# Kernel optimization log

Hardware: AMD Instinct MI355X
Metric: run time of the kernel (lower is better)

## Reference

```python
import jax, jax.numpy as jnp
import numpy as np

DIM = 1024
NUM_HEADS = 16
HEAD_DIM = DIM // NUM_HEADS
SCALE = DIM ** (-0.5)  # NOTE: original scales by full dim, not head_dim


def setup_inputs() -> dict:
    key = jax.random.key(0)
    ks = jax.random.split(key, 5)
    B, S = 2, 2048
    x = jax.random.normal(ks[0], (B, S, DIM), dtype=jnp.float32)
    w_qkv = jax.random.normal(ks[1], (DIM, 3 * DIM), dtype=jnp.float32) * (DIM ** -0.5)
    b_qkv = jax.random.normal(ks[2], (3 * DIM,), dtype=jnp.float32) * 0.02
    w_proj = jax.random.normal(ks[3], (DIM, DIM), dtype=jnp.float32) * (DIM ** -0.5)
    b_proj = jax.random.normal(ks[4], (DIM,), dtype=jnp.float32) * 0.02
    return {"x": x, "w_qkv": w_qkv, "b_qkv": b_qkv, "w_proj": w_proj, "b_proj": b_proj}


def reference(x, w_qkv, b_qkv, w_proj, b_proj):
    B, S, D = x.shape
    qkv = x @ w_qkv + b_qkv                                  # [B,S,3D]
    qkv = qkv.reshape(B, S, NUM_HEADS, 3 * HEAD_DIM).transpose(0, 2, 1, 3)  # [B,H,S,3hd]
    q, k, v = jnp.split(qkv, 3, axis=-1)                     # each [B,H,S,hd]
    attn = jnp.einsum("bhqd,bhkd->bhqk", q, k) * SCALE       # [B,H,S,S]
    attn = jax.nn.softmax(attn, axis=-1)
    out = jnp.einsum("bhqk,bhkd->bhqd", attn, v)             # [B,H,S,hd]
    out = out.transpose(0, 2, 1, 3).reshape(B, S, D)
    return out @ w_proj + b_proj
```

## Files before the change

kernel.cpp:

```cpp
#include <hip/hip_runtime.h>
#include <hip/hip_bf16.h>

#define DIM 1024
#define NH 16
#define HD 64
#define BB 2
#define SS 2048
#define MROWS (BB * SS)
#define SC_LOG2E 0.04508422002778011f

typedef unsigned short u16;
typedef unsigned int u32;
typedef __attribute__((ext_vector_type(8))) short short8;
typedef __attribute__((ext_vector_type(4))) float f32x4;

__device__ __forceinline__ u16 f2bf(float f) {
  union { float f; u32 u; } v; v.f = f;
  return (u16)((v.u + 0x7fffu + ((v.u >> 16) & 1u)) >> 16);
}

__device__ __forceinline__ u32 pack2bf(float a, float b) {
  union { __hip_bfloat162 h; u32 u; } cv;
  cv.h = __float22bfloat162_rn(make_float2(a, b));
  return cv.u;
}

__device__ __forceinline__ void async16(const u16* g, u16* l) {
  __builtin_amdgcn_global_load_lds(
      (const __attribute__((address_space(1))) void*)(const void*)g,
      (__attribute__((address_space(3))) void*)(void*)l, 16, 0, 0);
}

__device__ __forceinline__ short8 ld8(const u16* p) { return *(const short8*)p; }

__global__ void cvt_kernel(const float* __restrict__ in, u16* __restrict__ out, int n4) {
  int i = blockIdx.x * blockDim.x + threadIdx.x;
  if (i < n4) {
    float4 v = ((const float4*)in)[i];
    u32 lo = (u32)f2bf(v.x) | ((u32)f2bf(v.y) << 16);
    u32 hi = (u32)f2bf(v.z) | ((u32)f2bf(v.w) << 16);
    ((uint2*)out)[i] = make_uint2(lo, hi);
  }
}

__global__ void tconv_kernel(const float* __restrict__ in, u16* __restrict__ out, int R, int C) {
  __shared__ u16 t[64 * 65];
  int c0 = blockIdx.x * 64, r0 = blockIdx.y * 64;
  #pragma unroll
  for (int i = 0; i < 16; i++) {
    int j = i * 256 + threadIdx.x;
    int rr = j >> 6, cc = j & 63;
    t[rr * 65 + cc] = f2bf(in[(size_t)(r0 + rr) * C + c0 + cc]);
  }
  __syncthreads();
  #pragma unroll
  for (int i = 0; i < 16; i++) {
    int j = i * 256 + threadIdx.x;
    int oc = j >> 6, orr = j & 63;
    out[(size_t)(c0 + oc) * R + r0 + orr] = t[orr * 65 + oc];
  }
}

template <int MODE>
__global__ __launch_bounds__(256, 2) void gemm_bt(
    const u16* __restrict__ A, const u16* __restrict__ Bt,
    const float* __restrict__ bias, void* __restrict__ C,
    u16* __restrict__ vT, int M, int N, int K) {
  __shared__ __align__(16) u16 As[128 * 32];
  __shared__ __align__(16) u16 Bs[128 * 32];
  const int tid = threadIdx.x;
  const int w = tid >> 6, l = tid & 63;
  const int r = l & 15, q = l >> 4;
  const int m0 = blockIdx.y * 128, n0 = blockIdx.x * 128;
  const int qm = (w & 1) * 64, qn = (w >> 1) * 64;

  const size_t aoff = (size_t)(m0 + w * 16 + (l >> 2)) * K + (size_t)(l & 3) * 8;
  const size_t boff = (size_t)(n0 + w * 16 + (l >> 2)) * K + (size_t)(l & 3) * 8;
  u16* alds = &As[(w * 64 + l) * 8];
  u16* blds = &Bs[(w * 64 + l) * 8];

  f32x4 acc[4][4] = {};
  for (int k0 = 0; k0 < K; k0 += 32) {
    async16(A + aoff + k0, alds);
    async16(A + aoff + (size_t)64 * K + k0, alds + 2048);
    async16(Bt + boff + k0, blds);
    async16(Bt + boff + (size_t)64 * K + k0, blds + 2048);
    __syncthreads();
    short8 af[4], bfr[4];
    #pragma unroll
    for (int i = 0; i < 4; i++) af[i] = ld8(&As[(qm + i * 16 + r) * 32 + q * 8]);
    #pragma unroll
    for (int j = 0; j < 4; j++) bfr[j] = ld8(&Bs[(qn + j * 16 + r) * 32 + q * 8]);
    #pragma unroll
    for (int i = 0; i < 4; i++)
      #pragma unroll
      for (int j = 0; j < 4; j++)
        acc[i][j] = __builtin_amdgcn_mfma_f32_16x16x32_bf16(af[i], bfr[j], acc[i][j], 0, 0, 0);
    __syncthreads();
  }
  #pragma unroll
  for (int i = 0; i < 4; i++) {
    int ro = m0 + qm + i * 16 + q * 4;
    #pragma unroll
    for (int j = 0; j < 4; j++) {
      int col = n0 + qn + j * 16 + r;
      float bv = bias[col];
      float v0 = acc[i][j][0] + bv, v1 = acc[i][j][1] + bv;
      float v2 = acc[i][j][2] + bv, v3 = acc[i][j][3] + bv;
      if (MODE == 1) {
        float* out = (float*)C;
        out[(size_t)(ro + 0) * N + col] = v0;
        out[(size_t)(ro + 1) * N + col] = v1;
        out[(size_t)(ro + 2) * N + col] = v2;
        out[(size_t)(ro + 3) * N + col] = v3;
      } else {
        int h = col / 192, wi = col - h * 192;
        if (wi >= 128) {
          int bb = ro >> 11, s = ro & 2047, d = wi - 128;
          uint2 pk = make_uint2(pack2bf(v0, v1), pack2bf(v2, v3));
          *(uint2*)&vT[((size_t)((bb * NH + h) * HD + d)) * SS + s] = pk;
        } else {
          if (wi < 64) { v0 *= SC_LOG2E; v1 *= SC_LOG2E; v2 *= SC_LOG2E; v3 *= SC_LOG2E; }
          u16* qk2 = (u16*)C;
          qk2[(size_t)(ro + 0) * 2048 + h * 128 + wi] = f2bf(v0);
          qk2[(size_t)(ro + 1) * 2048 + h * 128 + wi] = f2bf(v1);
          qk2[(size_t)(ro + 2) * 2048 + h * 128 + wi] = f2bf(v2);
          qk2[(size_t)(ro + 3) * 2048 + h * 128 + wi] = f2bf(v3);
        }
      }
    }
  }
}

__global__ __launch_bounds__(256, 3) void attn4_kernel(
    const u16* __restrict__ qk2, const u16* __restrict__ vT,
    u16* __restrict__ attno) {
  __shared__ __align__(16) u16 Ks[128 * 64];
  __shared__ __align__(16) u16 Vs[64 * 128];
  __shared__ __align__(16) u16 pb[4][16 * 136];
  const int tid = threadIdx.x;
  const int w = tid >> 6, l = tid & 63;
  const int r = l & 15, q = l >> 4;
  const int b = blockIdx.z, h = blockIdx.y, q0 = blockIdx.x * 64;

  const u16* qb = qk2 + (size_t)b * SS * 2048;
  const u16* kB = qb + h * 128 + 64;
  const u16* vB = vT + (size_t)((b * NH + h) * HD) * SS;
  u16* pw = &pb[w][0];

  short8 qf[2];
  #pragma unroll
  for (int kq = 0; kq < 2; kq++)
    qf[kq] = ld8(qb + (size_t)(q0 + w * 16 + r) * 2048 + h * 128 + kq * 32 + q * 8);

  short8 ones;
  #pragma unroll
  for (int e = 0; e < 8; e++) ones[e] = (short)0x3F80;

  const int klrow = l >> 3;
  const int kchunk = (l & 7) ^ klrow;
  const int vlrow = l >> 4;
  const int vslot = l & 15;

  f32x4 oacc[4] = {};
  f32x4 dacc = {};

  for (int kv0 = 0; kv0 < SS; kv0 += 128) {
    #pragma unroll
    for (int t = 0; t < 4; t++) {
      int sl = (w * 4 + t) * 8 + klrow;
      async16(kB + (size_t)(kv0 + sl) * 2048 + kchunk * 8, &Ks[(w * 4 + t) * 512 + l * 8]);
    }
    #pragma unroll
    for (int t = 0; t < 4; t++) {
      int d = (w * 4 + t) * 4 + vlrow;
      int c = vslot ^ (t * 4 + vlrow);
      async16(vB + (size_t)d * SS + kv0 + c * 8, &Vs[(w * 4 + t) * 512 + l * 8]);
    }
    __syncthreads();

    f32x4 sacc[8] = {};
    #pragma unroll
    for (int j = 0; j < 8; j++) {
      int sl = j * 16 + r;
      short8 a0 = ld8(&Ks[sl * 64 + ((q ^ (r & 7)) * 8)]);
      short8 a1 = ld8(&Ks[sl * 64 + (((4 + q) ^ (r & 7)) * 8)]);
      sacc[j] = __builtin_amdgcn_mfma_f32_16x16x32_bf16(a0, qf[0], sacc[j], 0, 0, 0);
      sacc[j] = __builtin_amdgcn_mfma_f32_16x16x32_bf16(a1, qf[1], sacc[j], 0, 0, 0);
    }
    #pragma unroll
    for (int j = 0; j < 8; j++) {
      float p0 = __builtin_exp2f(sacc[j][0]);
      float p1 = __builtin_exp2f(sacc[j][1]);
      float p2 = __builtin_exp2f(sacc[j][2]);
      float p3 = __builtin_exp2f(sacc[j][3]);
      uint2 pk = make_uint2(pack2bf(p0, p1), pack2bf(p2, p3));
      *(uint2*)&pw[r * 136 + j * 16 + q * 4] = pk;
    }
    #pragma unroll
    for (int ks = 0; ks < 4; ks++) {
      short8 pa = ld8(&pw[r * 136 + ks * 32 + q * 8]);
      dacc = __builtin_amdgcn_mfma_f32_16x16x32_bf16(pa, ones, dacc, 0, 0, 0);
      #pragma unroll
      for (int dj = 0; dj < 4; dj++) {
        short8 vb = ld8(&Vs[(dj * 16 + r) * 128 + (((ks * 4 + q) ^ r) * 8)]);
        oacc[dj] = __builtin_amdgcn_mfma_f32_16x16x32_bf16(pa, vb, oacc[dj], 0, 0, 0);
      }
    }
    __syncthreads();
  }
  #pragma unroll
  for (int e = 0; e < 4; e++) {
    float di = 1.f / dacc[e];
    int row = q0 + w * 16 + q * 4 + e;
    #pragma unroll
    for (int dj = 0; dj < 4; dj++)
      attno[(size_t)(b * SS + row) * DIM + h * HD + dj * 16 + r] =
          f2bf(oacc[dj][e] * di);
  }
}

extern "C" void kernel_launch(void* const* d_in, const int* in_sizes, int n_in,
                              void* d_out, int out_size, void* d_ws, size_t ws_size,
                              hipStream_t stream) {
  const float* x      = (const float*)d_in[0];
  const float* w_qkv  = (const float*)d_in[1];
  const float* b_qkv  = (const float*)d_in[2];
  const float* w_proj = (const float*)d_in[3];
  const float* b_proj = (const float*)d_in[4];
  float* out = (float*)d_out;
  char* ws = (char*)d_ws;
  u16* xb     = (u16*)(ws);
  u16* wqkvT  = (u16*)(ws + ((size_t)8  << 20));
  u16* wprojT = (u16*)(ws + ((size_t)14 << 20));
  u16* qk2    = (u16*)(ws + ((size_t)16 << 20));
  u16* attno  = (u16*)(ws + ((size_t)32 << 20));
  u16* vT     = (u16*)(ws + ((size_t)40 << 20));

  cvt_kernel<<<4096, 256, 0, stream>>>(x, xb, MROWS * DIM / 4);
  tconv_kernel<<<dim3(48, 16), 256, 0, stream>>>(w_qkv, wqkvT, DIM, 3 * DIM);
  tconv_kernel<<<dim3(16, 16), 256, 0, stream>>>(w_proj, wprojT, DIM, DIM);
  gemm_bt<0><<<dim3(24, 32), 256, 0, stream>>>(xb, wqkvT, b_qkv, qk2, vT, MROWS, 3 * DIM, DIM);
  attn4_kernel<<<dim3(32, NH, BB), 256, 0, stream>>>(qk2, vT, attno);
  gemm_bt<1><<<dim3(8, 32), 256, 0, stream>>>(attno, wprojT, b_proj, out, nullptr, MROWS, DIM, DIM);
}
```

Baseline: 215.7 us.

## Store Q/K/V in MFMA fragment layout and split attention KV across two blocks

The QKV GEMM epilogue now writes Q, K and V straight into MFMA-fragment-ordered buffers, so the attention kernel loads contiguous 512-element fragments with no swizzle. The attention kernel now has each wave process 32 query rows, reusing each K/V fragment across two query tiles. The KV range is split in half across two blocks that combine unnormalized partial outputs and denominators with float atomics. Extra zero and reduce kernels are added, the output buffer is reused as scratch, and the atomics make the floating-point sum order nondeterministic.

```diff
diff --git a/kernel.cpp b/kernel.cpp
--- a/kernel.cpp
+++ b/kernel.cpp
@@ -65,12 +65,12 @@
 __global__ __launch_bounds__(256, 2) void gemm_bt(
     const u16* __restrict__ A, const u16* __restrict__ Bt,
     const float* __restrict__ bias, void* __restrict__ C,
-    u16* __restrict__ vT, int M, int N, int K) {
+    u16* __restrict__ kF, u16* __restrict__ vF, int M, int N, int K) {
   __shared__ __align__(16) u16 As[128 * 32];
   __shared__ __align__(16) u16 Bs[128 * 32];
   const int tid = threadIdx.x;
   const int w = tid >> 6, l = tid & 63;
-  const int r = l & 15, q = l >> 4;
+  const int r = l & 15, qd = l >> 4;
   const int m0 = blockIdx.y * 128, n0 = blockIdx.x * 128;
   const int qm = (w & 1) * 64, qn = (w >> 1) * 64;
 
@@ -88,9 +88,9 @@
     __syncthreads();
     short8 af[4], bfr[4];
     #pragma unroll
-    for (int i = 0; i < 4; i++) af[i] = ld8(&As[(qm + i * 16 + r) * 32 + q * 8]);
-    #pragma unroll
-    for (int j = 0; j < 4; j++) bfr[j] = ld8(&Bs[(qn + j * 16 + r) * 32 + q * 8]);
+    for (int i = 0; i < 4; i++) af[i] = ld8(&As[(qm + i * 16 + r) * 32 + qd * 8]);
+    #pragma unroll
+    for (int j = 0; j < 4; j++) bfr[j] = ld8(&Bs[(qn + j * 16 + r) * 32 + qd * 8]);
     #pragma unroll
     for (int i = 0; i < 4; i++)
       #pragma unroll
@@ -100,124 +100,165 @@
   }
   #pragma unroll
   for (int i = 0; i < 4; i++) {
-    int ro = m0 + qm + i * 16 + q * 4;
+    int ro = m0 + qm + i * 16 + qd * 4;
     #pragma unroll
     for (int j = 0; j < 4; j++) {
-      int col = n0 + qn + j * 16 + r;
-      float bv = bias[col];
+      int cb = n0 + qn + j * 16;
+      float bv = bias[cb + r];
       float v0 = acc[i][j][0] + bv, v1 = acc[i][j][1] + bv;
       float v2 = acc[i][j][2] + bv, v3 = acc[i][j][3] + bv;
       if (MODE == 1) {
         float* out = (float*)C;
+        int col = cb + r;
         out[(size_t)(ro + 0) * N + col] = v0;
         out[(size_t)(ro + 1) * N + col] = v1;
         out[(size_t)(ro + 2) * N + col] = v2;
         out[(size_t)(ro + 3) * N + col] = v3;
       } else {
-        int h = col / 192, wi = col - h * 192;
-        if (wi >= 128) {
-          int bb = ro >> 11, s = ro & 2047, d = wi - 128;
+        int h = cb / 192, wib = cb - h * 192;
+        int bb = ro >> 11, s = ro & 2047;
+        int bh = bb * 16 + h;
+        if (wib < 128) {
+          int d = (wib & 63) + r;
+          u16* dst = (wib < 64) ? (u16*)C : kF;
+          if (wib < 64) { v0 *= SC_LOG2E; v1 *= SC_LOG2E; v2 *= SC_LOG2E; v3 *= SC_LOG2E; }
+          size_t fr = ((size_t)bh * 128 + (s >> 4)) * 2 + (d >> 5);
+          size_t bo = fr * 512 + (size_t)((d & 31) >> 3) * 128 + (d & 7) + (size_t)qd * 32;
+          dst[bo + 0]  = f2bf(v0);
+          dst[bo + 8]  = f2bf(v1);
+          dst[bo + 16] = f2bf(v2);
+          dst[bo + 24] = f2bf(v3);
+        } else {
+          int d = (wib - 128) + r;
+          size_t fr = ((size_t)bh * 64 + (s >> 5)) * 4 + (d >> 4);
+          int lb = r + 16 * ((i & 1) * 2 + (qd >> 1));
           uint2 pk = make_uint2(pack2bf(v0, v1), pack2bf(v2, v3));
-          *(uint2*)&vT[((size_t)((bb * NH + h) * HD + d)) * SS + s] = pk;
-        } else {
-          if (wi < 64) { v0 *= SC_LOG2E; v1 *= SC_LOG2E; v2 *= SC_LOG2E; v3 *= SC_LOG2E; }
-          u16* qk2 = (u16*)C;
-          qk2[(size_t)(ro + 0) * 2048 + h * 128 + wi] = f2bf(v0);
-          qk2[(size_t)(ro + 1) * 2048 + h * 128 + wi] = f2bf(v1);
-          qk2[(size_t)(ro + 2) * 2048 + h * 128 + wi] = f2bf(v2);
-          qk2[(size_t)(ro + 3) * 2048 + h * 128 + wi] = f2bf(v3);
+          *(uint2*)&vF[fr * 512 + (size_t)lb * 8 + (qd & 1) * 4] = pk;
         }
       }
     }
   }
 }
 
-__global__ __launch_bounds__(256, 3) void attn4_kernel(
-    const u16* __restrict__ qk2, const u16* __restrict__ vT,
-    u16* __restrict__ attno) {
-  __shared__ __align__(16) u16 Ks[128 * 64];
-  __shared__ __align__(16) u16 Vs[64 * 128];
-  __shared__ __align__(16) u16 pb[4][16 * 136];
+__global__ void zero_kernel(float4* __restrict__ po4, float4* __restrict__ dl4) {
+  int i = blockIdx.x * 256 + threadIdx.x;
+  float4 z = {0.f, 0.f, 0.f, 0.f};
+  if (i < (MROWS * NH * HD / 4)) po4[i] = z;
+  if (i < (MROWS * NH / 4)) dl4[i] = z;
+}
+
+__global__ __launch_bounds__(256, 3) void attn5_kernel(
+    const u16* __restrict__ qF, const u16* __restrict__ kF,
+    const u16* __restrict__ vF, float* __restrict__ po,
+    float* __restrict__ dl) {
+  __shared__ __align__(16) u16 Ks[16 * 512];
+  __shared__ __align__(16) u16 Vs[16 * 512];
+  __shared__ __align__(16) u16 Ps[4][2 * 512];
   const int tid = threadIdx.x;
   const int w = tid >> 6, l = tid & 63;
-  const int r = l & 15, q = l >> 4;
-  const int b = blockIdx.z, h = blockIdx.y, q0 = blockIdx.x * 64;
-
-  const u16* qb = qk2 + (size_t)b * SS * 2048;
-  const u16* kB = qb + h * 128 + 64;
-  const u16* vB = vT + (size_t)((b * NH + h) * HD) * SS;
-  u16* pw = &pb[w][0];
-
-  short8 qf[2];
-  #pragma unroll
-  for (int kq = 0; kq < 2; kq++)
-    qf[kq] = ld8(qb + (size_t)(q0 + w * 16 + r) * 2048 + h * 128 + kq * 32 + q * 8);
+  const int r = l & 15, qd = l >> 4;
+  const int half = blockIdx.x & 1, qblk = blockIdx.x >> 1;
+  const int bh = blockIdx.z * NH + blockIdx.y;
+  const int q0 = qblk * 128;
+
+  const u16* qFb = qF + (size_t)bh * 128 * 2 * 512;
+  const u16* kFb = kF + (size_t)bh * 128 * 2 * 512;
+  const u16* vFb = vF + (size_t)bh * 64 * 4 * 512;
+  u16* pw = &Ps[w][0];
+  const int pwo = r * 8 + (qd >> 1) * 128 + (qd & 1) * 4;
+
+  short8 qf[2][2];
+  #pragma unroll
+  for (int i = 0; i < 2; i++)
+    #pragma unroll
+    for (int kd = 0; kd < 2; kd++)
+      qf[i][kd] = ld8(qFb + ((size_t)((q0 >> 4) + w * 2 + i) * 2 + kd) * 512 + l * 8);
 
   short8 ones;
   #pragma unroll
   for (int e = 0; e < 8; e++) ones[e] = (short)0x3F80;
 
-  const int klrow = l >> 3;
-  const int kchunk = (l & 7) ^ klrow;
-  const int vlrow = l >> 4;
-  const int vslot = l & 15;
-
-  f32x4 oacc[4] = {};
-  f32x4 dacc = {};
-
-  for (int kv0 = 0; kv0 < SS; kv0 += 128) {
+  f32x4 oacc[2][4] = {};
+  f32x4 dacc[2] = {};
+
+  const int kvend = half * 1024 + 1024;
+  for (int kv0 = half * 1024; kv0 < kvend; kv0 += 128) {
+    const u16* ksrc = kFb + (size_t)(kv0 >> 4) * 2 * 512;
+    const u16* vsrc = vFb + (size_t)(kv0 >> 5) * 4 * 512;
     #pragma unroll
     for (int t = 0; t < 4; t++) {
-      int sl = (w * 4 + t) * 8 + klrow;
-      async16(kB + (size_t)(kv0 + sl) * 2048 + kchunk * 8, &Ks[(w * 4 + t) * 512 + l * 8]);
-    }
-    #pragma unroll
-    for (int t = 0; t < 4; t++) {
-      int d = (w * 4 + t) * 4 + vlrow;
-      int c = vslot ^ (t * 4 + vlrow);
-      async16(vB + (size_t)d * SS + kv0 + c * 8, &Vs[(w * 4 + t) * 512 + l * 8]);
-    }
-    __syncthreads();
-
-    f32x4 sacc[8] = {};
-    #pragma unroll
-    for (int j = 0; j < 8; j++) {
-      int sl = j * 16 + r;
-      short8 a0 = ld8(&Ks[sl * 64 + ((q ^ (r & 7)) * 8)]);
-      short8 a1 = ld8(&Ks[sl * 64 + (((4 + q) ^ (r & 7)) * 8)]);
-      sacc[j] = __builtin_amdgcn_mfma_f32_16x16x32_bf16(a0, qf[0], sacc[j], 0, 0, 0);
-      sacc[j] = __builtin_amdgcn_mfma_f32_16x16x32_bf16(a1, qf[1], sacc[j], 0, 0, 0);
-    }
-    #pragma unroll
-    for (int j = 0; j < 8; j++) {
-      float p0 = __builtin_exp2f(sacc[j][0]);
-      float p1 = __builtin_exp2f(sacc[j][1]);
-      float p2 = __builtin_exp2f(sacc[j][2]);
-      float p3 = __builtin_exp2f(sacc[j][3]);
-      uint2 pk = make_uint2(pack2bf(p0, p1), pack2bf(p2, p3));
-      *(uint2*)&pw[r * 136 + j * 16 + q * 4] = pk;
-    }
+      int fi = w * 4 + t;
+      async16(ksrc + fi * 512 + l * 8, &Ks[fi * 512 + l * 8]);
+      async16(vsrc + fi * 512 + l * 8, &Vs[fi * 512 + l * 8]);
+    }
+    __syncthreads();
+
     #pragma unroll
     for (int ks = 0; ks < 4; ks++) {
-      short8 pa = ld8(&pw[r * 136 + ks * 32 + q * 8]);
-      dacc = __builtin_amdgcn_mfma_f32_16x16x32_bf16(pa, ones, dacc, 0, 0, 0);
+      short8 a00 = ld8(&Ks[(ks * 4 + 0) * 512 + l * 8]);
+      short8 a01 = ld8(&Ks[(ks * 4 + 1) * 512 + l * 8]);
+      short8 a10 = ld8(&Ks[(ks * 4 + 2) * 512 + l * 8]);
+      short8 a11 = ld8(&Ks[(ks * 4 + 3) * 512 + l * 8]);
+      f32x4 s00 = {}, s01 = {}, s10 = {}, s11 = {};
+      s00 = __builtin_amdgcn_mfma_f32_16x16x32_bf16(a00, qf[0][0], s00, 0, 0, 0);
+      s00 = __builtin_amdgcn_mfma_f32_16x16x32_bf16(a01, qf[0][1], s00, 0, 0, 0);
+      s01 = __builtin_amdgcn_mfma_f32_16x16x32_bf16(a00, qf[1][0], s01, 0, 0, 0);
+      s01 = __builtin_amdgcn_mfma_f32_16x16x32_bf16(a01, qf[1][1], s01, 0, 0, 0);
+      s10 = __builtin_amdgcn_mfma_f32_16x16x32_bf16(a10, qf[0][0], s10, 0, 0, 0);
+      s10 = __builtin_amdgcn_mfma_f32_16x16x32_bf16(a11, qf[0][1], s10, 0, 0, 0);
+      s11 = __builtin_amdgcn_mfma_f32_16x16x32_bf16(a10, qf[1][0], s11, 0, 0, 0);
+      s11 = __builtin_amdgcn_mfma_f32_16x16x32_bf16(a11, qf[1][1], s11, 0, 0, 0);
+      {
+        uint2 pk;
+        pk = make_uint2(pack2bf(__builtin_exp2f(s00[0]), __builtin_exp2f(s00[1])),
+                        pack2bf(__builtin_exp2f(s00[2]), __builtin_exp2f(s00[3])));
+        *(uint2*)&pw[0 * 512 + pwo + 0 * 256] = pk;
+        pk = make_uint2(pack2bf(__builtin_exp2f(s01[0]), __builtin_exp2f(s01[1])),
+                        pack2bf(__builtin_exp2f(s01[2]), __builtin_exp2f(s01[3])));
+        *(uint2*)&pw[1 * 512 + pwo + 0 * 256] = pk;
+        pk = make_uint2(pack2bf(__builtin_exp2f(s10[0]), __builtin_exp2f(s10[1])),
+                        pack2bf(__builtin_exp2f(s10[2]), __builtin_exp2f(s10[3])));
+        *(uint2*)&pw[0 * 512 + pwo + 1 * 256] = pk;
+        pk = make_uint2(pack2bf(__builtin_exp2f(s11[0]), __builtin_exp2f(s11[1])),
+                        pack2bf(__builtin_exp2f(s11[2]), __builtin_exp2f(s11[3])));
+        *(uint2*)&pw[1 * 512 + pwo + 1 * 256] = pk;
+      }
+      short8 pa0 = ld8(&pw[0 * 512 + l * 8]);
+      short8 pa1 = ld8(&pw[1 * 512 + l * 8]);
+      dacc[0] = __builtin_amdgcn_mfma_f32_16x16x32_bf16(pa0, ones, dacc[0], 0, 0, 0);
+      dacc[1] = __builtin_amdgcn_mfma_f32_16x16x32_bf16(pa1, ones, dacc[1], 0, 0, 0);
       #pragma unroll
       for (int dj = 0; dj < 4; dj++) {
-        short8 vb = ld8(&Vs[(dj * 16 + r) * 128 + (((ks * 4 + q) ^ r) * 8)]);
-        oacc[dj] = __builtin_amdgcn_mfma_f32_16x16x32_bf16(pa, vb, oacc[dj], 0, 0, 0);
+        short8 vb = ld8(&Vs[(ks * 4 + dj) * 512 + l * 8]);
+        oacc[0][dj] = __builtin_amdgcn_mfma_f32_16x16x32_bf16(pa0, vb, oacc[0][dj], 0, 0, 0);
+        oacc[1][dj] = __builtin_amdgcn_mfma_f32_16x16x32_bf16(pa1, vb, oacc[1][dj], 0, 0, 0);
       }
     }
     __syncthreads();
   }
   #pragma unroll
-  for (int e = 0; e < 4; e++) {
-    float di = 1.f / dacc[e];
-    int row = q0 + w * 16 + q * 4 + e;
-    #pragma unroll
-    for (int dj = 0; dj < 4; dj++)
-      attno[(size_t)(b * SS + row) * DIM + h * HD + dj * 16 + r] =
-          f2bf(oacc[dj][e] * di);
-  }
+  for (int i = 0; i < 2; i++)
+    #pragma unroll
+    for (int e = 0; e < 4; e++) {
+      int row = q0 + w * 32 + i * 16 + qd * 4 + e;
+      float* pr = po + ((size_t)bh * SS + row) * HD;
+      #pragma unroll
+      for (int dj = 0; dj < 4; dj++)
+        atomicAdd(pr + dj * 16 + r, oacc[i][dj][e]);
+      if (r == 0) atomicAdd(dl + (size_t)bh * SS + row, dacc[i][e]);
+    }
+}
+
+__global__ void reduce_kernel(const float* __restrict__ po, const float* __restrict__ dl,
+                              u16* __restrict__ attno) {
+  int i = blockIdx.x * 256 + threadIdx.x;
+  int row = i >> 4, dg = i & 15;
+  int bh = row >> 11, s = row & 2047;
+  int b = bh >> 4, h = bh & 15;
+  float4 o = ((const float4*)po)[i];
+  float inv = 1.f / dl[row];
+  uint2 pk = make_uint2(pack2bf(o.x * inv, o.y * inv), pack2bf(o.z * inv, o.w * inv));
+  *(uint2*)&attno[(size_t)(b * SS + s) * DIM + h * HD + dg * 4] = pk;
 }
 
 extern "C" void kernel_launch(void* const* d_in, const int* in_sizes, int n_in,
@@ -230,17 +271,22 @@
   const float* b_proj = (const float*)d_in[4];
   float* out = (float*)d_out;
   char* ws = (char*)d_ws;
-  u16* xb     = (u16*)(ws);
-  u16* wqkvT  = (u16*)(ws + ((size_t)8  << 20));
-  u16* wprojT = (u16*)(ws + ((size_t)14 << 20));
-  u16* qk2    = (u16*)(ws + ((size_t)16 << 20));
-  u16* attno  = (u16*)(ws + ((size_t)32 << 20));
-  u16* vT     = (u16*)(ws + ((size_t)40 << 20));
+  u16* qF     = (u16*)(ws);
+  u16* kF     = (u16*)(ws + ((size_t)8  << 20));
+  u16* vF     = (u16*)(ws + ((size_t)16 << 20));
+  u16* wprojT = (u16*)(ws + ((size_t)24 << 20));
+  u16* attno  = (u16*)(ws + ((size_t)26 << 20));
+  u16* xb     = (u16*)(ws + ((size_t)34 << 20));
+  u16* wqkvT  = (u16*)(ws + ((size_t)42 << 20));
+  float* dl   = (float*)(ws + ((size_t)34 << 20));
+  float* po   = out;
 
   cvt_kernel<<<4096, 256, 0, stream>>>(x, xb, MROWS * DIM / 4);
   tconv_kernel<<<dim3(48, 16), 256, 0, stream>>>(w_qkv, wqkvT, DIM, 3 * DIM);
   tconv_kernel<<<dim3(16, 16), 256, 0, stream>>>(w_proj, wprojT, DIM, DIM);
-  gemm_bt<0><<<dim3(24, 32), 256, 0, stream>>>(xb, wqkvT, b_qkv, qk2, vT, MROWS, 3 * DIM, DIM);
-  attn4_kernel<<<dim3(32, NH, BB), 256, 0, stream>>>(qk2, vT, attno);
-  gemm_bt<1><<<dim3(8, 32), 256, 0, stream>>>(attno, wprojT, b_proj, out, nullptr, MROWS, DIM, DIM);
-}
+  gemm_bt<0><<<dim3(24, 32), 256, 0, stream>>>(xb, wqkvT, b_qkv, qF, kF, vF, MROWS, 3 * DIM, DIM);
+  zero_kernel<<<4096, 256, 0, stream>>>((float4*)po, (float4*)dl);
+  attn5_kernel<<<dim3(32, NH, BB), 256, 0, stream>>>(qF, kF, vF, po, dl);
+  reduce_kernel<<<4096, 256, 0, stream>>>(po, dl, attno);
+  gemm_bt<1><<<dim3(8, 32), 256, 0, stream>>>(attno, wprojT, b_proj, out, nullptr, nullptr, MROWS, DIM, DIM);
+}
```

Measured after the change: 227.1 us. 1.05x slower.
